# Performance work log

Measured on AMD Instinct MI355X. Metric: run time of the kernel, lower is better.

## Reference

```python
import jax, jax.numpy as jnp
import numpy as np

PH, PW, SR = 7, 7, 2  # aligned_height, aligned_width, sampling_ratio


def setup_inputs() -> dict:
    key = jax.random.key(0)
    k1, k2, k3, k4 = jax.random.split(key, 4)
    B, C, H, W, N = 2, 256, 200, 200, 1000
    features = jax.random.normal(k1, (B, C, H, W), dtype=jnp.float32)
    # build valid boxes [x1, y1, x2, y2] in feature-map pixel coords
    ctr = jax.random.uniform(k2, (N, 2), minval=0.0, maxval=float(W))
    half = jax.random.uniform(k3, (N, 2), minval=2.0, maxval=50.0)
    xy1 = jnp.clip(ctr - half, 0.0, float(W) - 1.0)
    xy2 = jnp.clip(ctr + half, 0.0, float(W) - 1.0)
    rois = jnp.concatenate([xy1, xy2], axis=1).astype(jnp.float32)  # [N,4]
    sample_indices = jax.random.randint(k4, (N,), 0, B).astype(jnp.int32)
    return {"features": features, "rois": rois, "sample_indices": sample_indices}


def _roi_align(features, rois, sample_indices):
    B, C, H, W = features.shape
    N = rois.shape[0]
    feats = jnp.transpose(features, (0, 2, 3, 1))  # [B,H,W,C] for gather locality
    x1, y1, x2, y2 = rois[:, 0], rois[:, 1], rois[:, 2], rois[:, 3]
    roi_w = jnp.maximum(x2 - x1, 1.0)
    roi_h = jnp.maximum(y2 - y1, 1.0)
    bin_h = roi_h / PH
    bin_w = roi_w / PW
    g = SR
    # sample point t in [0, PH*g): y = y1 + (t + 0.5)/g * bin_h (Detectron grid)
    ty = (jnp.arange(PH * g, dtype=jnp.float32) + 0.5) / g  # [PH*g]
    tx = (jnp.arange(PW * g, dtype=jnp.float32) + 0.5) / g  # [PW*g]
    ys = y1[:, None] + ty[None, :] * bin_h[:, None]  # [N, PH*g]
    xs = x1[:, None] + tx[None, :] * bin_w[:, None]  # [N, PW*g]
    valid_y = (ys >= -1.0) & (ys <= H)
    valid_x = (xs >= -1.0) & (xs <= W)
    yc = jnp.clip(ys, 0.0, H - 1.0)
    xc = jnp.clip(xs, 0.0, W - 1.0)
    y0 = jnp.floor(yc).astype(jnp.int32)
    x0 = jnp.floor(xc).astype(jnp.int32)
    y1i = jnp.minimum(y0 + 1, H - 1)
    x1i = jnp.minimum(x0 + 1, W - 1)
    ly = yc - y0.astype(jnp.float32)  # [N, PH*g]
    lx = xc - x0.astype(jnp.float32)  # [N, PW*g]
    hy, hx = 1.0 - ly, 1.0 - lx
    b = sample_indices.astype(jnp.int32)[:, None, None]  # [N,1,1]
    Y0, Y1 = y0[:, :, None], y1i[:, :, None]              # [N,Th,1]
    X0, X1 = x0[:, None, :], x1i[:, None, :]              # [N,1,Tw]
    # bilinear weights, zeroed outside the valid range (kernel semantics)
    mask = (valid_y[:, :, None] & valid_x[:, None, :]).astype(feats.dtype)
    w00 = (hy[:, :, None] * hx[:, None, :] * mask)[..., None]
    w01 = (hy[:, :, None] * lx[:, None, :] * mask)[..., None]
    w10 = (ly[:, :, None] * hx[:, None, :] * mask)[..., None]
    w11 = (ly[:, :, None] * lx[:, None, :] * mask)[..., None]
    vals = (w00 * feats[b, Y0, X0]
            + w01 * feats[b, Y0, X1]
            + w10 * feats[b, Y1, X0]
            + w11 * feats[b, Y1, X1])  # [N, PH*g, PW*g, C]
    out = vals.reshape(N, PH, g, PW, g, C).mean(axis=(2, 4))  # avg over samples
    return jnp.transpose(out, (0, 3, 1, 2))  # [N, C, PH, PW]


def reference(features, rois, sample_indices):
    return _roi_align(features, rois, sample_indices)
```

## Files before the change

### kernel.cpp

```cpp
#include <hip/hip_runtime.h>

#define CCH 256
#define HH 200
#define WW 200
#define HWW (HH * WW)
#define PHB 7
#define PWB 7
#define NBINS 49
#define OUTSZ (CCH * NBINS)

typedef float f4v __attribute__((ext_vector_type(4)));
typedef unsigned short us4 __attribute__((ext_vector_type(4)));

__device__ __forceinline__ unsigned short f2bf(float f) {
  unsigned u = __builtin_bit_cast(unsigned, f);
  u += 0x7fffu + ((u >> 16) & 1u);
  return (unsigned short)(u >> 16);
}
__device__ __forceinline__ float bf_lo(unsigned u) {
  return __builtin_bit_cast(float, u << 16);
}
__device__ __forceinline__ float bf_hi(unsigned u) {
  return __builtin_bit_cast(float, u & 0xffff0000u);
}

__global__ __launch_bounds__(256) void transpose_kernel(
    const float* __restrict__ in, unsigned short* __restrict__ out) {
  __shared__ float tile[64][65];
  const int b  = blockIdx.z;
  const int p0 = blockIdx.x * 64;
  const int c0 = blockIdx.y * 64;
  const int t  = threadIdx.x;
  const int k  = t & 15;
  const int r0 = t >> 4;
  const float* ip = in  + (size_t)b * CCH * HWW;
  unsigned short* op = out + (size_t)b * HWW * CCH;
#pragma unroll
  for (int rr = 0; rr < 4; ++rr) {
    const int c = r0 + rr * 16;
    const f4v v = __builtin_nontemporal_load(
        (const f4v*)(ip + (size_t)(c0 + c) * HWW + p0 + 4 * k));
    tile[c][4 * k + 0] = v.x;
    tile[c][4 * k + 1] = v.y;
    tile[c][4 * k + 2] = v.z;
    tile[c][4 * k + 3] = v.w;
  }
  __syncthreads();
#pragma unroll
  for (int rr = 0; rr < 4; ++rr) {
    const int p = r0 + rr * 16;
    us4 v;
    v.x = f2bf(tile[4 * k + 0][p]);
    v.y = f2bf(tile[4 * k + 1][p]);
    v.z = f2bf(tile[4 * k + 2][p]);
    v.w = f2bf(tile[4 * k + 3][p]);
    *(us4*)(op + (size_t)(p0 + p) * CCH + c0 + 4 * k) = v;
  }
}

__global__ __launch_bounds__(256) void roi_kernel(
    const unsigned short* __restrict__ feat, const float* __restrict__ rois,
    const int* __restrict__ sidx, float* __restrict__ out) {
  __shared__ float s_out[128 * NBINS];
  __shared__ int   s_yi[2][14];
  __shared__ int   s_xi[2][14];
  __shared__ float s_ly[14], s_hy[14], s_vy[14];
  __shared__ float s_lx[14], s_hx[14], s_vx[14];

  const int n = blockIdx.x >> 1;
  const int h = blockIdx.x & 1;
  const int t = threadIdx.x;

  const float x1 = rois[n * 4 + 0];
  const float y1 = rois[n * 4 + 1];
  const float x2 = rois[n * 4 + 2];
  const float y2 = rois[n * 4 + 3];
  const int   bb = sidx[n];
  const float bin_w = fmaxf(x2 - x1, 1.0f) / 7.0f;
  const float bin_h = fmaxf(y2 - y1, 1.0f) / 7.0f;

  if (t < 14) {
    const float tt = ((float)t + 0.5f) * 0.5f;
    const float ys = y1 + tt * bin_h;
    s_vy[t] = (ys >= -1.0f && ys <= (float)HH) ? 1.0f : 0.0f;
    const float yc  = fminf(fmaxf(ys, 0.0f), (float)(HH - 1));
    const int   yy0 = (int)yc;
    const int   yy1 = min(yy0 + 1, HH - 1);
    const float ly  = yc - (float)yy0;
    s_yi[0][t] = yy0 * WW;
    s_yi[1][t] = yy1 * WW;
    s_ly[t] = ly;
    s_hy[t] = 1.0f - ly;
  } else if (t < 28) {
    const int   i  = t - 14;
    const float tt = ((float)i + 0.5f) * 0.5f;
    const float xs = x1 + tt * bin_w;
    s_vx[i] = (xs >= -1.0f && xs <= (float)WW) ? 1.0f : 0.0f;
    const float xc  = fminf(fmaxf(xs, 0.0f), (float)(WW - 1));
    const int   xx0 = (int)xc;
    const int   xx1 = min(xx0 + 1, WW - 1);
    const float lx  = xc - (float)xx0;
    s_xi[0][i] = xx0;
    s_xi[1][i] = xx1;
    s_lx[i] = lx;
    s_hx[i] = 1.0f - lx;
  }
  __syncthreads();

  const int lane = t & 63;
  const int wv   = t >> 6;
  const unsigned short* Fb = feat + (size_t)bb * HWW * CCH + 128 * h + 2 * lane;

#pragma unroll 2
  for (int bin = wv; bin < NBINS; bin += 4) {
    const int ph = bin / PWB;
    const int pw = bin - ph * PWB;
    float accx = 0.0f, accy = 0.0f;
#pragma unroll
    for (int sy = 0; sy < 2; ++sy) {
      const int   iy  = ph * 2 + sy;
      const int   yr0 = s_yi[0][iy];
      const int   yr1 = s_yi[1][iy];
      const float ly  = s_ly[iy];
      const float hy  = s_hy[iy];
      const float vy  = s_vy[iy];
#pragma unroll
      for (int sx = 0; sx < 2; ++sx) {
        const int   ix  = pw * 2 + sx;
        const int   xx0 = s_xi[0][ix];
        const int   xx1 = s_xi[1][ix];
        const float m   = vy * s_vx[ix];
        const float w00 = m * s_hx[ix] * hy;
        const float w01 = m * s_lx[ix] * hy;
        const float w10 = m * s_hx[ix] * ly;
        const float w11 = m * s_lx[ix] * ly;
        const unsigned q00 = *(const unsigned*)(Fb + (size_t)(yr0 + xx0) * CCH);
        const unsigned q01 = *(const unsigned*)(Fb + (size_t)(yr0 + xx1) * CCH);
        const unsigned q10 = *(const unsigned*)(Fb + (size_t)(yr1 + xx0) * CCH);
        const unsigned q11 = *(const unsigned*)(Fb + (size_t)(yr1 + xx1) * CCH);
        accx += w00 * bf_lo(q00) + w01 * bf_lo(q01) +
                w10 * bf_lo(q10) + w11 * bf_lo(q11);
        accy += w00 * bf_hi(q00) + w01 * bf_hi(q01) +
                w10 * bf_hi(q10) + w11 * bf_hi(q11);
      }
    }
    s_out[(2 * lane + 0) * NBINS + bin] = accx * 0.25f;
    s_out[(2 * lane + 1) * NBINS + bin] = accy * 0.25f;
  }
  __syncthreads();

  const f4v* so4 = (const f4v*)s_out;
  f4v*       on4 = (f4v*)(out + (size_t)n * OUTSZ + 128 * h * NBINS);
  for (int i = t; i < (128 * NBINS) / 4; i += 256) on4[i] = so4[i];
}

__global__ __launch_bounds__(256) void roi_kernel_nchw(
    const float* __restrict__ feat, const float* __restrict__ rois,
    const int* __restrict__ sidx, float* __restrict__ out) {
  __shared__ float s_out[OUTSZ];
  __shared__ int   s_yi[2][14];
  __shared__ int   s_xi[2][14];
  __shared__ float s_ly[14], s_hy[14], s_vy[14];
  __shared__ float s_lx[14], s_hx[14], s_vx[14];
  const int n = blockIdx.x;
  const int t = threadIdx.x;
  const float x1 = rois[n * 4 + 0], y1 = rois[n * 4 + 1];
  const float x2 = rois[n * 4 + 2], y2 = rois[n * 4 + 3];
  const int   bb = sidx[n];
  const float bin_w = fmaxf(x2 - x1, 1.0f) / 7.0f;
  const float bin_h = fmaxf(y2 - y1, 1.0f) / 7.0f;
  if (t < 14) {
    const float tt = ((float)t + 0.5f) * 0.5f;
    const float ys = y1 + tt * bin_h;
    s_vy[t] = (ys >= -1.0f && ys <= (float)HH) ? 1.0f : 0.0f;
    const float yc = fminf(fmaxf(ys, 0.0f), (float)(HH - 1));
    const int yy0 = (int)yc, yy1 = min(yy0 + 1, HH - 1);
    s_yi[0][t] = yy0 * WW; s_yi[1][t] = yy1 * WW;
    s_ly[t] = yc - (float)yy0; s_hy[t] = 1.0f - s_ly[t];
  } else if (t < 28) {
    const int i = t - 14;
    const float tt = ((float)i + 0.5f) * 0.5f;
    const float xs = x1 + tt * bin_w;
    s_vx[i] = (xs >= -1.0f && xs <= (float)WW) ? 1.0f : 0.0f;
    const float xc = fminf(fmaxf(xs, 0.0f), (float)(WW - 1));
    const int xx0 = (int)xc, xx1 = min(xx0 + 1, WW - 1);
    s_xi[0][i] = xx0; s_xi[1][i] = xx1;
    s_lx[i] = xc - (float)xx0; s_hx[i] = 1.0f - s_lx[i];
  }
  __syncthreads();
  const int c = t;
  const float* Fb = feat + ((size_t)bb * CCH + c) * HWW;
  for (int bin = 0; bin < NBINS; ++bin) {
    const int ph = bin / PWB, pw = bin - ph * PWB;
    float acc = 0.0f;
    for (int sy = 0; sy < 2; ++sy) {
      const int iy = ph * 2 + sy;
      for (int sx = 0; sx < 2; ++sx) {
        const int ix = pw * 2 + sx;
        const float m = s_vy[iy] * s_vx[ix];
        acc += m * (s_hy[iy] * (s_hx[ix] * Fb[s_yi[0][iy] + s_xi[0][ix]] +
                                s_lx[ix] * Fb[s_yi[0][iy] + s_xi[1][ix]]) +
                    s_ly[iy] * (s_hx[ix] * Fb[s_yi[1][iy] + s_xi[0][ix]] +
                                s_lx[ix] * Fb[s_yi[1][iy] + s_xi[1][ix]]));
      }
    }
    s_out[c * NBINS + bin] = acc * 0.25f;
  }
  __syncthreads();
  float* on = out + (size_t)n * OUTSZ;
  for (int i = t; i < OUTSZ; i += 256) on[i] = s_out[i];
}

extern "C" void kernel_launch(void* const* d_in, const int* in_sizes, int n_in,
                              void* d_out, int out_size, void* d_ws, size_t ws_size,
                              hipStream_t stream) {
  const float* features = (const float*)d_in[0];
  const float* rois     = (const float*)d_in[1];
  const int*   sidx     = (const int*)d_in[2];
  float*       out      = (float*)d_out;

  const int N = in_sizes[1] / 4;
  const int B = in_sizes[0] / (CCH * HWW);

  const size_t need = (size_t)B * HWW * CCH * sizeof(unsigned short);
  if (ws_size >= need) {
    unsigned short* ft = (unsigned short*)d_ws;
    dim3 tgrid(HWW / 64, CCH / 64, B);
    transpose_kernel<<<tgrid, 256, 0, stream>>>(features, ft);
    roi_kernel<<<2 * N, 256, 0, stream>>>(ft, rois, sidx, out);
  } else {
    roi_kernel_nchw<<<N, 256, 0, stream>>>(features, rois, sidx, out);
  }
}
```

Before: 176.9 us.

## Precompute per-sample bilinear tap table and use 8-byte loads, two bins per wave

Replaces the separate per-axis shared arrays with a 196-entry table of precomputed byte offsets and pre-scaled weights, one per sample point, built in parallel by 196 threads. Each lane now loads 8 bytes (4 bf16 channels) per tap, so half a wave covers the 128-channel slice and each wave processes two bins at once. This cuts load instruction count and per-sample weight arithmetic. The cost is some idle work on the padded 50th bin and 4-way shared stores with possible bank conflicts.

Result: no change. 175.4 us (-0.9%).

```diff
diff --git a/kernel.cpp b/kernel.cpp
--- a/kernel.cpp
+++ b/kernel.cpp
@@ -11,6 +11,8 @@
 
 typedef float f4v __attribute__((ext_vector_type(4)));
 typedef unsigned short us4 __attribute__((ext_vector_type(4)));
+typedef unsigned u2v __attribute__((ext_vector_type(2)));
+typedef unsigned u4v __attribute__((ext_vector_type(4)));
 
 __device__ __forceinline__ unsigned short f2bf(float f) {
   unsigned u = __builtin_bit_cast(unsigned, f);
@@ -58,94 +60,98 @@
   }
 }
 
+struct __align__(16) Tap {
+  unsigned off[4];
+  float    w[4];
+};
+
 __global__ __launch_bounds__(256) void roi_kernel(
     const unsigned short* __restrict__ feat, const float* __restrict__ rois,
     const int* __restrict__ sidx, float* __restrict__ out) {
   __shared__ float s_out[128 * NBINS];
-  __shared__ int   s_yi[2][14];
-  __shared__ int   s_xi[2][14];
-  __shared__ float s_ly[14], s_hy[14], s_vy[14];
-  __shared__ float s_lx[14], s_hx[14], s_vx[14];
+  __shared__ Tap   s_tab[196];
 
   const int n = blockIdx.x >> 1;
   const int h = blockIdx.x & 1;
   const int t = threadIdx.x;
-
-  const float x1 = rois[n * 4 + 0];
-  const float y1 = rois[n * 4 + 1];
-  const float x2 = rois[n * 4 + 2];
-  const float y2 = rois[n * 4 + 3];
-  const int   bb = sidx[n];
-  const float bin_w = fmaxf(x2 - x1, 1.0f) / 7.0f;
-  const float bin_h = fmaxf(y2 - y1, 1.0f) / 7.0f;
-
-  if (t < 14) {
-    const float tt = ((float)t + 0.5f) * 0.5f;
-    const float ys = y1 + tt * bin_h;
-    s_vy[t] = (ys >= -1.0f && ys <= (float)HH) ? 1.0f : 0.0f;
-    const float yc  = fminf(fmaxf(ys, 0.0f), (float)(HH - 1));
-    const int   yy0 = (int)yc;
-    const int   yy1 = min(yy0 + 1, HH - 1);
-    const float ly  = yc - (float)yy0;
-    s_yi[0][t] = yy0 * WW;
-    s_yi[1][t] = yy1 * WW;
-    s_ly[t] = ly;
-    s_hy[t] = 1.0f - ly;
-  } else if (t < 28) {
-    const int   i  = t - 14;
-    const float tt = ((float)i + 0.5f) * 0.5f;
-    const float xs = x1 + tt * bin_w;
-    s_vx[i] = (xs >= -1.0f && xs <= (float)WW) ? 1.0f : 0.0f;
-    const float xc  = fminf(fmaxf(xs, 0.0f), (float)(WW - 1));
-    const int   xx0 = (int)xc;
-    const int   xx1 = min(xx0 + 1, WW - 1);
-    const float lx  = xc - (float)xx0;
-    s_xi[0][i] = xx0;
-    s_xi[1][i] = xx1;
-    s_lx[i] = lx;
-    s_hx[i] = 1.0f - lx;
+  const int bb = sidx[n];
+
+  if (t < 196) {
+    const float x1 = rois[n * 4 + 0];
+    const float y1 = rois[n * 4 + 1];
+    const float x2 = rois[n * 4 + 2];
+    const float y2 = rois[n * 4 + 3];
+    const float bin_w = fmaxf(x2 - x1, 1.0f) * (1.0f / 7.0f);
+    const float bin_h = fmaxf(y2 - y1, 1.0f) * (1.0f / 7.0f);
+    const int iy = t / 14;
+    const int ix = t - iy * 14;
+    const float ys = y1 + ((float)iy + 0.5f) * 0.5f * bin_h;
+    const float xs = x1 + ((float)ix + 0.5f) * 0.5f * bin_w;
+    const float vy = (ys >= -1.0f && ys <= (float)HH) ? 1.0f : 0.0f;
+    const float vx = (xs >= -1.0f && xs <= (float)WW) ? 1.0f : 0.0f;
+    const float yc = fminf(fmaxf(ys, 0.0f), (float)(HH - 1));
+    const float xc = fminf(fmaxf(xs, 0.0f), (float)(WW - 1));
+    const int yy0 = (int)yc;
+    const int xx0 = (int)xc;
+    const int yy1 = min(yy0 + 1, HH - 1);
+    const int xx1 = min(xx0 + 1, WW - 1);
+    const float ly = yc - (float)yy0, hy = 1.0f - ly;
+    const float lx = xc - (float)xx0, hx = 1.0f - lx;
+    const float f = vy * vx * 0.25f;
+    const unsigned r0 = (unsigned)(yy0 * WW);
+    const unsigned r1 = (unsigned)(yy1 * WW);
+    s_tab[t].off[0] = (r0 + (unsigned)xx0) * (CCH * 2);
+    s_tab[t].off[1] = (r0 + (unsigned)xx1) * (CCH * 2);
+    s_tab[t].off[2] = (r1 + (unsigned)xx0) * (CCH * 2);
+    s_tab[t].off[3] = (r1 + (unsigned)xx1) * (CCH * 2);
+    s_tab[t].w[0] = f * hy * hx;
+    s_tab[t].w[1] = f * hy * lx;
+    s_tab[t].w[2] = f * ly * hx;
+    s_tab[t].w[3] = f * ly * lx;
   }
   __syncthreads();
 
   const int lane = t & 63;
   const int wv   = t >> 6;
-  const unsigned short* Fb = feat + (size_t)bb * HWW * CCH + 128 * h + 2 * lane;
-
-#pragma unroll 2
-  for (int bin = wv; bin < NBINS; bin += 4) {
-    const int ph = bin / PWB;
-    const int pw = bin - ph * PWB;
-    float accx = 0.0f, accy = 0.0f;
+  const unsigned laneoff = (unsigned)((lane & 31) << 3);
+  const char* __restrict__ base =
+      (const char*)feat + ((size_t)bb * HWW * CCH + 128 * h) * 2;
+
+  for (int p = wv; p < 25; p += 4) {
+    const int mybin = 2 * p + (lane >> 5);
+    const int bin   = min(mybin, NBINS - 1);
+    const int ph  = bin / PWB;
+    const int pw  = bin - ph * PWB;
+    const int s00 = (2 * ph) * 14 + 2 * pw;
+    float a0 = 0.0f, a1 = 0.0f, a2 = 0.0f, a3 = 0.0f;
 #pragma unroll
     for (int sy = 0; sy < 2; ++sy) {
-      const int   iy  = ph * 2 + sy;
-      const int   yr0 = s_yi[0][iy];
-      const int   yr1 = s_yi[1][iy];
-      const float ly  = s_ly[iy];
-      const float hy  = s_hy[iy];
-      const float vy  = s_vy[iy];
 #pragma unroll
       for (int sx = 0; sx < 2; ++sx) {
-        const int   ix  = pw * 2 + sx;
-        const int   xx0 = s_xi[0][ix];
-        const int   xx1 = s_xi[1][ix];
-        const float m   = vy * s_vx[ix];
-        const float w00 = m * s_hx[ix] * hy;
-        const float w01 = m * s_lx[ix] * hy;
-        const float w10 = m * s_hx[ix] * ly;
-        const float w11 = m * s_lx[ix] * ly;
-        const unsigned q00 = *(const unsigned*)(Fb + (size_t)(yr0 + xx0) * CCH);
-        const unsigned q01 = *(const unsigned*)(Fb + (size_t)(yr0 + xx1) * CCH);
-        const unsigned q10 = *(const unsigned*)(Fb + (size_t)(yr1 + xx0) * CCH);
-        const unsigned q11 = *(const unsigned*)(Fb + (size_t)(yr1 + xx1) * CCH);
-        accx += w00 * bf_lo(q00) + w01 * bf_lo(q01) +
-                w10 * bf_lo(q10) + w11 * bf_lo(q11);
-        accy += w00 * bf_hi(q00) + w01 * bf_hi(q01) +
-                w10 * bf_hi(q10) + w11 * bf_hi(q11);
+        const Tap* tp = &s_tab[s00 + sy * 14 + sx];
+        const u4v o4 = *(const u4v*)tp->off;
+        const f4v w4 = *(const f4v*)tp->w;
+        const u2v q00 = *(const u2v*)(base + (o4.x + laneoff));
+        const u2v q01 = *(const u2v*)(base + (o4.y + laneoff));
+        const u2v q10 = *(const u2v*)(base + (o4.z + laneoff));
+        const u2v q11 = *(const u2v*)(base + (o4.w + laneoff));
+        a0 += w4.x * bf_lo(q00.x) + w4.y * bf_lo(q01.x)
+            + w4.z * bf_lo(q10.x) + w4.w * bf_lo(q11.x);
+        a1 += w4.x * bf_hi(q00.x) + w4.y * bf_hi(q01.x)
+            + w4.z * bf_hi(q10.x) + w4.w * bf_hi(q11.x);
+        a2 += w4.x * bf_lo(q00.y) + w4.y * bf_lo(q01.y)
+            + w4.z * bf_lo(q10.y) + w4.w * bf_lo(q11.y);
+        a3 += w4.x * bf_hi(q00.y) + w4.y * bf_hi(q01.y)
+            + w4.z * bf_hi(q10.y) + w4.w * bf_hi(q11.y);
       }
     }
-    s_out[(2 * lane + 0) * NBINS + bin] = accx * 0.25f;
-    s_out[(2 * lane + 1) * NBINS + bin] = accy * 0.25f;
+    if (mybin < NBINS) {
+      const int c0 = (lane & 31) << 2;
+      s_out[(c0 + 0) * NBINS + mybin] = a0;
+      s_out[(c0 + 1) * NBINS + mybin] = a1;
+      s_out[(c0 + 2) * NBINS + mybin] = a2;
+      s_out[(c0 + 3) * NBINS + mybin] = a3;
+    }
   }
   __syncthreads();
 
```
